# Optimization experiments

Measured on AMD Instinct MI355X. Metric: run time of the kernel, lower is better.

Reference implementation:

```python
import jax, jax.numpy as jnp
import numpy as np

B, DV, DT, H, G, E = 4096, 1024, 1024, 1024, 4096, 8
D = DV + DT  # fused dim = 2048


def setup_inputs() -> dict:
    key = jax.random.key(0)
    ks = jax.random.split(key, 8)
    s = 0.02
    return {
        "vision_cls": jax.random.normal(ks[0], (B, DV), jnp.float32),
        "text_cls": jax.random.normal(ks[1], (B, DT), jnp.float32),
        "W1_imm": jax.random.normal(ks[2], (E, D, H), jnp.float32) * s,
        "b1_imm": jnp.zeros((E, H), jnp.float32),
        "W2_imm": jax.random.normal(ks[3], (E, H, 1), jnp.float32) * s,
        "b2_imm": jnp.zeros((E, 1), jnp.float32),
        "W1_gene": jax.random.normal(ks[4], (E, D, H), jnp.float32) * s,
        "b1_gene": jnp.zeros((E, H), jnp.float32),
        "W2_gene": jax.random.normal(ks[5], (E, H, G), jnp.float32) * s,
        "b2_gene": jnp.zeros((E, G), jnp.float32),
        "organ_idx": jax.random.randint(ks[6], (B,), 0, E, jnp.int32),
    }


def reference(vision_cls, text_cls, W1_imm, b1_imm, W2_imm, b2_imm,
              W1_gene, b1_gene, W2_gene, b2_gene, organ_idx):
    # fused features [B, D]
    fused = jnp.concatenate([vision_cls, text_cls], axis=-1)
    # Dense MoE reference: run every organ head on the full batch, then
    # select each sample's routed output (same math as the per-group
    # gather -> MLP -> scatter in the original; dropout is eval-mode identity).
    h_i = jax.nn.relu(jnp.einsum('bd,edh->ebh', fused, W1_imm) + b1_imm[:, None, :])
    imm_all = jnp.einsum('ebh,eh->eb', h_i, W2_imm[:, :, 0]) + b2_imm[:, :1]  # [E,B]
    h_g = jax.nn.relu(jnp.einsum('bd,edh->ebh', fused, W1_gene) + b1_gene[:, None, :])
    gene_all = jnp.einsum('ebh,ehg->ebg', h_g, W2_gene) + b2_gene[:, None, :]  # [E,B,G]
    bidx = jnp.arange(fused.shape[0])
    immune = imm_all[organ_idx, bidx]      # [B]
    gene = gene_all[organ_idx, bidx]       # [B,G] (uniform gene_dim -> no padding needed)
    return immune, gene, vision_cls, text_cls
```

## Files before the change

kernel.cpp:

```cpp
#include <hip/hip_runtime.h>


#define B_N 4096
#define DV  1024
#define DD  2048
#define HH  1024
#define GG  4096
#define EE  8
#define BM  128
#define MAXRB 40
#define PERM_N (MAXRB * BM)

typedef __bf16 bf16x8 __attribute__((ext_vector_type(8)));
typedef float f32x4 __attribute__((ext_vector_type(4)));
typedef unsigned short u16x4v __attribute__((ext_vector_type(4)));
typedef unsigned short u16x8v __attribute__((ext_vector_type(8)));

#define H_CNT 0
#define H_FIL 8
#define H_OFF 16
#define H_NRB 24
#define H_BLK 32

static __device__ __forceinline__ unsigned short f2bf(float f) {
  return __builtin_bit_cast(unsigned short, (__bf16)f);
}
static __device__ __forceinline__ float bf2f(unsigned short s) {
  return __builtin_bit_cast(float, (unsigned)s << 16);
}
static __device__ __forceinline__ void gload16(const void* g, void* l) {
  __builtin_amdgcn_global_load_lds(
      (const __attribute__((address_space(1))) unsigned int*)g,
      (__attribute__((address_space(3))) unsigned int*)l, 16, 0, 0);
}

__global__ __launch_bounds__(1024) void routing(const int* __restrict__ organ,
                                                int* __restrict__ hdr,
                                                int* __restrict__ perm) {
  __shared__ int cnt[EE], fil[EE], off[EE];
  const int tid = threadIdx.x;
  if (tid < EE) { cnt[tid] = 0; fil[tid] = 0; }
  __syncthreads();
#pragma unroll
  for (int i = 0; i < 4; ++i) atomicAdd(&cnt[organ[tid + (i << 10)]], 1);
#pragma unroll
  for (int i = 0; i < 5; ++i) perm[tid + (i << 10)] = -1;
  __syncthreads();
  if (tid == 0) {
    int acc = 0;
    for (int e = 0; e < EE; ++e) {
      off[e] = acc;
      hdr[H_OFF + e] = acc;
      hdr[H_CNT + e] = cnt[e];
      int nb = (cnt[e] + BM - 1) >> 7;
      int rb0 = acc >> 7;
      for (int i = 0; i < nb; ++i) hdr[H_BLK + rb0 + i] = e;
      acc += nb << 7;
    }
    hdr[H_NRB] = acc >> 7;
  }
  __syncthreads();
#pragma unroll
  for (int i = 0; i < 4; ++i) {
    int b = tid + (i << 10);
    int e = organ[b];
    int slot = off[e] + atomicAdd(&fil[e], 1);
    perm[slot] = b;
  }
}

static __device__ __forceinline__ void abuild_body(
    int bx, const float* __restrict__ vis, const float* __restrict__ txt,
    const int* __restrict__ hdr, const int* __restrict__ perm,
    unsigned short* __restrict__ Abuf) {
  const int nr = hdr[H_NRB] << 7;
  const int tid = threadIdx.x;
  const int c = tid << 3;
  const float* srcbase = (c < DV) ? vis : txt;
  const int cc = (c < DV) ? c : c - DV;
#pragma unroll
  for (int p = 0; p < 4; ++p) {
    int r = (bx << 2) + p;
    if (r >= nr) return;
    int smp = perm[r];
    u16x8v v;
    if (smp >= 0) {
      const float* src = srcbase + (size_t)smp * 1024 + cc;
      float4 a = *(const float4*)src, b = *(const float4*)(src + 4);
      v[0] = f2bf(a.x); v[1] = f2bf(a.y); v[2] = f2bf(a.z); v[3] = f2bf(a.w);
      v[4] = f2bf(b.x); v[5] = f2bf(b.y); v[6] = f2bf(b.z); v[7] = f2bf(b.w);
    } else {
#pragma unroll
      for (int i = 0; i < 8; ++i) v[i] = 0;
    }
    *(u16x8v*)&Abuf[(size_t)r * DD + c] = v;
  }
}

static __device__ __forceinline__ void copy_body(
    int bx, const float4* __restrict__ v, const float4* __restrict__ t,
    float4* __restrict__ ov, float4* __restrict__ ot) {
  const int n4 = B_N * DV / 4;
  for (int i = bx * 256 + (int)threadIdx.x; i < n4; i += 1024 * 256) {
    ov[i] = v[i];
    ot[i] = t[i];
  }
}

__global__ __launch_bounds__(256) void k_A(
    const float* __restrict__ vis, const float* __restrict__ txt,
    const int* __restrict__ hdr, const int* __restrict__ perm,
    unsigned short* __restrict__ Abuf, float4* __restrict__ ov,
    float4* __restrict__ ot) {
  int bx = blockIdx.x;
  if (bx < PERM_N / 4) { abuild_body(bx, vis, txt, hdr, perm, Abuf); return; }
  bx -= PERM_N / 4;
  copy_body(bx, (const float4*)vis, (const float4*)txt, ov, ot);
}

template <int KDIM, int NST>
static __device__ __forceinline__ void gemm_core(
    const unsigned short* __restrict__ Aseg,
    const float* __restrict__ Bglob,
    unsigned short* smem, f32x4 (&acc)[4][4]) {
  const int tid = threadIdx.x;
  const int lane = tid & 63;
  const int wr = ((tid >> 6) >> 1) << 6, wc = ((tid >> 6) & 1) << 6;
  const int lr = lane & 15, lk = (lane >> 4) << 3;
  const int arow = tid >> 2, akq = (tid & 3) << 3;
  const int wbase = (tid & 192) << 3;
  const int bn = tid & 127, bkh = tid >> 7;
  const int bs3 = (bn ^ (bn >> 3)) & 7;
  constexpr int NT = KDIM / 32;

  float bv[16];

  auto issueA = [&](int buf, int k0) {
    gload16(Aseg + (size_t)arow * KDIM + k0 + akq, smem + (buf << 12) + wbase);
    gload16(Aseg + (size_t)(64 + arow) * KDIM + k0 + akq,
            smem + (buf << 12) + 2048 + wbase);
  };
  auto issueB = [&](int k0) {
    const float* p = Bglob + (size_t)(k0 + (bkh << 4)) * NST + bn;
#pragma unroll
    for (int i = 0; i < 16; ++i) bv[i] = p[(size_t)i * NST];
  };
  auto writeB = [&](int buf) {
    unsigned short* row = smem + 8192 + (buf << 12) + (bn << 5);
#pragma unroll
    for (int j = 0; j < 4; ++j) {
      u16x4v w;
      w[0] = f2bf(bv[4 * j + 0]);
      w[1] = f2bf(bv[4 * j + 1]);
      w[2] = f2bf(bv[4 * j + 2]);
      w[3] = f2bf(bv[4 * j + 3]);
      *(u16x4v*)(row + ((((bkh << 2) + j) ^ bs3) << 2)) = w;
    }
  };

  issueA(0, 0);
  issueB(0);
  writeB(0);
  asm volatile("s_waitcnt vmcnt(0)" ::: "memory");
  __syncthreads();

#pragma unroll 2
  for (int kt = 0; kt < NT; ++kt) {
    const int cur = kt & 1;
    if (kt + 1 < NT) {
      issueA(cur ^ 1, (kt + 1) << 5);
      issueB((kt + 1) << 5);
    }
    bf16x8 af[4], bfr[4];
#pragma unroll
    for (int m = 0; m < 4; ++m)
      af[m] = *(const bf16x8*)&smem[(cur << 12) + (wr + m * 16 + lr) * 32 + lk];
#pragma unroll
    for (int n = 0; n < 4; ++n) {
      const int fr = wc + n * 16 + lr;
      const int s3 = (fr ^ (fr >> 3)) & 7;
      const unsigned short* row = smem + 8192 + (cur << 12) + (fr << 5);
      const int g = (lane >> 4) << 1;
      union { unsigned long long q[2]; bf16x8 v; } u;
      u.q[0] = *(const unsigned long long*)(row + ((g ^ s3) << 2));
      u.q[1] = *(const unsigned long long*)(row + (((g + 1) ^ s3) << 2));
      bfr[n] = u.v;
    }
#pragma unroll
    for (int m = 0; m < 4; ++m)
#pragma unroll
      for (int n = 0; n < 4; ++n)
        acc[m][n] = __builtin_amdgcn_mfma_f32_16x16x32_bf16(af[m], bfr[n], acc[m][n], 0, 0, 0);
    if (kt + 1 < NT) writeB(cur ^ 1);
    asm volatile("s_waitcnt vmcnt(0)" ::: "memory");
    __syncthreads();
  }
}

__global__ __launch_bounds__(256) void k_L1(
    const unsigned short* __restrict__ Abuf, const float* __restrict__ W1i,
    const float* __restrict__ W1g, const float* __restrict__ b1i,
    const float* __restrict__ b1g, const int* __restrict__ hdr,
    unsigned short* __restrict__ H1, unsigned short* __restrict__ H2) {
  __shared__ __align__(16) unsigned short smem[16384];
  const int bx = blockIdx.x;
  const int rb = bx >> 4;
  if (rb >= hdr[H_NRB]) return;
  const int sub = bx & 15, head = sub >> 3, cb = (sub & 7) << 7;
  const int e = hdr[H_BLK + rb];
  const float* Bglob = (head ? W1g : W1i) + (size_t)e * DD * HH + cb;
  const float* bias = (head ? b1g : b1i) + e * HH;
  unsigned short* Hout = head ? H2 : H1;
  const int tid = threadIdx.x;
  const int lane = tid & 63, wave = tid >> 6;
  const int wr = (wave >> 1) << 6, wc = (wave & 1) << 6;
  const int lr = lane & 15;

  f32x4 acc[4][4];
#pragma unroll
  for (int m = 0; m < 4; ++m)
#pragma unroll
    for (int n = 0; n < 4; ++n) acc[m][n] = (f32x4){0.f, 0.f, 0.f, 0.f};

  gemm_core<DD, HH>(Abuf + (size_t)rb * BM * DD, Bglob, smem, acc);

  const int r0l = wr + ((lane >> 4) << 2);
#pragma unroll
  for (int n = 0; n < 4; ++n) {
    const int col = wc + n * 16 + lr;
    const float bv = bias[cb + col];
#pragma unroll
    for (int m = 0; m < 4; ++m)
#pragma unroll
      for (int v = 0; v < 4; ++v) {
        int row = r0l + m * 16 + v;
        float x = acc[m][n][v] + bv;
        x = x > 0.f ? x : 0.f;
        smem[((row << 7) + col) ^ ((row & 7) << 3)] = f2bf(x);
      }
  }
  __syncthreads();
#pragma unroll
  for (int c = 0; c < 8; ++c) {
    int q = c * 256 + tid;
    int row = q >> 4, ch = q & 15;
    int off = ((row << 7) + (ch << 3)) ^ ((row & 7) << 3);
    u16x8v val = *(const u16x8v*)&smem[off];
    *(u16x8v*)&Hout[(size_t)(rb * BM + row) * HH + cb + (ch << 3)] = val;
  }
}

static __device__ __forceinline__ void immune_body(
    int bx, const int* __restrict__ hdr, const int* __restrict__ perm,
    const unsigned short* __restrict__ H1, const float* __restrict__ W2,
    const float* __restrict__ b2, float* __restrict__ out) {
  const int nrb = hdr[H_NRB];
  const int r = bx * 4 + (threadIdx.x >> 6);
  if (r >= nrb * BM) return;
  const int b = perm[r];
  if (b < 0) return;
  const int e = hdr[H_BLK + (r >> 7)];
  const int lane = threadIdx.x & 63;
  const unsigned short* h = H1 + (size_t)r * HH + lane * 16;
  const float* w = W2 + (size_t)e * HH + lane * 16;
  float s = 0.f;
#pragma unroll
  for (int i = 0; i < 16; ++i) s += bf2f(h[i]) * w[i];
#pragma unroll
  for (int off = 32; off >= 1; off >>= 1) s += __shfl_xor(s, off, 64);
  if (lane == 0) out[b] = s + b2[e];
}

#define G_L2 (MAXRB * 32)
__global__ __launch_bounds__(256) void k_L2(
    const unsigned short* __restrict__ H2buf, const float* __restrict__ W2g,
    const float* __restrict__ b2g, const int* __restrict__ hdr,
    const int* __restrict__ perm, float* __restrict__ outg,
    const unsigned short* __restrict__ H1, const float* __restrict__ W2i,
    const float* __restrict__ b2i, float* __restrict__ outi) {
  __shared__ __align__(16) unsigned short smem[16384];
  int bx = blockIdx.x;
  if (bx >= G_L2) {
    immune_body(bx - G_L2, hdr, perm, H1, W2i, b2i, outi);
    return;
  }
  const int rb = bx % MAXRB;
  const int cb = (bx / MAXRB) << 7;
  if (rb >= hdr[H_NRB]) return;
  const int e = hdr[H_BLK + rb];
  const float* Bglob = W2g + (size_t)e * HH * GG + cb;
  const int tid = threadIdx.x;
  const int lane = tid & 63, wave = tid >> 6;
  const int wr = (wave >> 1) << 6, wc = (wave & 1) << 6;
  const int lr = lane & 15;

  f32x4 acc[4][4];
#pragma unroll
  for (int m = 0; m < 4; ++m)
#pragma unroll
    for (int n = 0; n < 4; ++n) acc[m][n] = (f32x4){0.f, 0.f, 0.f, 0.f};

  gemm_core<HH, GG>(H2buf + (size_t)rb * BM * HH, Bglob, smem, acc);

  const int r0l = wr + ((lane >> 4) << 2);
#pragma unroll
  for (int n = 0; n < 4; ++n) {
    const int col = wc + n * 16 + lr;
    const float bv = b2g[e * GG + cb + col];
#pragma unroll
    for (int m = 0; m < 4; ++m)
#pragma unroll
      for (int v = 0; v < 4; ++v) {
        int row = r0l + m * 16 + v;
        smem[((row << 7) + col) ^ ((row & 7) << 3)] = f2bf(acc[m][n][v] + bv);
      }
  }
  __syncthreads();
#pragma unroll
  for (int c = 0; c < 8; ++c) {
    int q = c * 256 + tid;
    int row = q >> 4, ch = q & 15;
    int sm = perm[rb * BM + row];
    if (sm < 0) continue;
    int off = ((row << 7) + (ch << 3)) ^ ((row & 7) << 3);
    u16x8v val = *(const u16x8v*)&smem[off];
    float4 f0, f1;
    f0.x = bf2f(val[0]); f0.y = bf2f(val[1]); f0.z = bf2f(val[2]); f0.w = bf2f(val[3]);
    f1.x = bf2f(val[4]); f1.y = bf2f(val[5]); f1.z = bf2f(val[6]); f1.w = bf2f(val[7]);
    float* dst = outg + (size_t)sm * GG + cb + (ch << 3);
    *(float4*)dst = f0;
    *(float4*)(dst + 4) = f1;
  }
}

extern "C" void kernel_launch(void* const* d_in, const int* in_sizes, int n_in,
                              void* d_out, int out_size, void* d_ws, size_t ws_size,
                              hipStream_t stream) {
  (void)in_sizes; (void)n_in; (void)out_size; (void)ws_size;
  const float* vis = (const float*)d_in[0];
  const float* txt = (const float*)d_in[1];
  const float* W1i = (const float*)d_in[2];
  const float* b1i = (const float*)d_in[3];
  const float* W2i = (const float*)d_in[4];
  const float* b2i = (const float*)d_in[5];
  const float* W1g = (const float*)d_in[6];
  const float* b1g = (const float*)d_in[7];
  const float* W2g = (const float*)d_in[8];
  const float* b2g = (const float*)d_in[9];
  const int* organ = (const int*)d_in[10];

  float* out_imm = (float*)d_out;
  float* out_gene = out_imm + B_N;
  float* out_vis = out_gene + (size_t)B_N * GG;
  float* out_txt = out_vis + (size_t)B_N * DV;

  int* hdr = (int*)d_ws;
  int* perm = hdr + 128;

  const size_t OFF_ABUF = 32768;
  const size_t OFF_H1 = OFF_ABUF + (size_t)PERM_N * DD * 2;
  const size_t OFF_H2 = OFF_H1 + (size_t)PERM_N * HH * 2;
  unsigned short* Abuf = (unsigned short*)((char*)d_ws + OFF_ABUF);
  unsigned short* H1 = (unsigned short*)((char*)d_ws + OFF_H1);
  unsigned short* H2 = (unsigned short*)((char*)d_ws + OFF_H2);

  routing<<<1, 1024, 0, stream>>>(organ, hdr, perm);
  k_A<<<PERM_N / 4 + 1024, 256, 0, stream>>>(vis, txt, hdr, perm, Abuf,
                                             (float4*)out_vis, (float4*)out_txt);
  k_L1<<<MAXRB * 16, 256, 0, stream>>>(Abuf, W1i, W1g, b1i, b1g, hdr, H1, H2);
  k_L2<<<G_L2 + PERM_N / 4, 256, 0, stream>>>(H2, W2g, b2g, hdr, perm, out_gene,
                                              H1, W2i, b2i, out_imm);
}
```

Before: 283.0 us.

## Deepen GEMM prefetch with register double-buffered B, swizzled A, block remap

Restructures the GEMM main loop so B tiles are fetched two K-steps ahead into alternating register buffers using float4 loads, and relaxes waits to vmcnt(4) so global loads stay in flight across barriers. It also XOR-swizzles A's LDS layout to reduce bank conflicts, and remaps block indices so consecutive blocks share the same expert weight column tile for better L2 reuse. The vis/txt output copy moves from the A-build kernel into the L1 kernel so it overlaps with GEMM work. The cost is more registers, hand-tuned waitcnt counts that must match the load count exactly, and an extra barrier before the epilogue.

```diff
diff --git a/kernel.cpp b/kernel.cpp
--- a/kernel.cpp
+++ b/kernel.cpp
@@ -69,10 +69,11 @@
   }
 }
 
-static __device__ __forceinline__ void abuild_body(
-    int bx, const float* __restrict__ vis, const float* __restrict__ txt,
+__global__ __launch_bounds__(256) void k_A(
+    const float* __restrict__ vis, const float* __restrict__ txt,
     const int* __restrict__ hdr, const int* __restrict__ perm,
     unsigned short* __restrict__ Abuf) {
+  const int bx = blockIdx.x;
   const int nr = hdr[H_NRB] << 7;
   const int tid = threadIdx.x;
   const int c = tid << 3;
@@ -107,17 +108,6 @@
   }
 }
 
-__global__ __launch_bounds__(256) void k_A(
-    const float* __restrict__ vis, const float* __restrict__ txt,
-    const int* __restrict__ hdr, const int* __restrict__ perm,
-    unsigned short* __restrict__ Abuf, float4* __restrict__ ov,
-    float4* __restrict__ ot) {
-  int bx = blockIdx.x;
-  if (bx < PERM_N / 4) { abuild_body(bx, vis, txt, hdr, perm, Abuf); return; }
-  bx -= PERM_N / 4;
-  copy_body(bx, (const float4*)vis, (const float4*)txt, ov, ot);
-}
-
 template <int KDIM, int NST>
 static __device__ __forceinline__ void gemm_core(
     const unsigned short* __restrict__ Aseg,
@@ -126,60 +116,54 @@
   const int tid = threadIdx.x;
   const int lane = tid & 63;
   const int wr = ((tid >> 6) >> 1) << 6, wc = ((tid >> 6) & 1) << 6;
-  const int lr = lane & 15, lk = (lane >> 4) << 3;
-  const int arow = tid >> 2, akq = (tid & 3) << 3;
+  const int lr = lane & 15;
+  const int arow = tid >> 2;
+  const int kq_src = (((tid & 3) ^ ((arow >> 1) & 3)) << 3);
   const int wbase = (tid & 192) << 3;
-  const int bn = tid & 127, bkh = tid >> 7;
-  const int bs3 = (bn ^ (bn >> 3)) & 7;
+  const int bn4 = (tid & 31) << 2;
+  const int bk4 = (tid >> 5) << 2;
   constexpr int NT = KDIM / 32;
 
-  float bv[16];
+  float4 bvA[4], bvB[4];
 
   auto issueA = [&](int buf, int k0) {
-    gload16(Aseg + (size_t)arow * KDIM + k0 + akq, smem + (buf << 12) + wbase);
-    gload16(Aseg + (size_t)(64 + arow) * KDIM + k0 + akq,
+    gload16(Aseg + (size_t)arow * KDIM + k0 + kq_src, smem + (buf << 12) + wbase);
+    gload16(Aseg + (size_t)(64 + arow) * KDIM + k0 + kq_src,
             smem + (buf << 12) + 2048 + wbase);
   };
-  auto issueB = [&](int k0) {
-    const float* p = Bglob + (size_t)(k0 + (bkh << 4)) * NST + bn;
-#pragma unroll
-    for (int i = 0; i < 16; ++i) bv[i] = p[(size_t)i * NST];
+  auto issueB = [&](float4 (&bv)[4], int k0) {
+    const float* p = Bglob + (size_t)(k0 + bk4) * NST + bn4;
+#pragma unroll
+    for (int i = 0; i < 4; ++i) bv[i] = *(const float4*)(p + (size_t)i * NST);
   };
-  auto writeB = [&](int buf) {
-    unsigned short* row = smem + 8192 + (buf << 12) + (bn << 5);
+  auto writeB = [&](int buf, float4 (&bv)[4]) {
+    const float* f0 = (const float*)&bv[0];
+    const float* f1 = (const float*)&bv[1];
+    const float* f2 = (const float*)&bv[2];
+    const float* f3 = (const float*)&bv[3];
 #pragma unroll
     for (int j = 0; j < 4; ++j) {
+      const int n = bn4 + j;
+      const int s3 = (n ^ (n >> 3)) & 7;
       u16x4v w;
-      w[0] = f2bf(bv[4 * j + 0]);
-      w[1] = f2bf(bv[4 * j + 1]);
-      w[2] = f2bf(bv[4 * j + 2]);
-      w[3] = f2bf(bv[4 * j + 3]);
-      *(u16x4v*)(row + ((((bkh << 2) + j) ^ bs3) << 2)) = w;
+      w[0] = f2bf(f0[j]); w[1] = f2bf(f1[j]);
+      w[2] = f2bf(f2[j]); w[3] = f2bf(f3[j]);
+      *(u16x4v*)(smem + 8192 + (buf << 12) + (n << 5) + ((((bk4 >> 2)) ^ s3) << 2)) = w;
     }
   };
-
-  issueA(0, 0);
-  issueB(0);
-  writeB(0);
-  asm volatile("s_waitcnt vmcnt(0)" ::: "memory");
-  __syncthreads();
-
-#pragma unroll 2
-  for (int kt = 0; kt < NT; ++kt) {
-    const int cur = kt & 1;
-    if (kt + 1 < NT) {
-      issueA(cur ^ 1, (kt + 1) << 5);
-      issueB((kt + 1) << 5);
-    }
+  auto compute = [&](int buf) {
     bf16x8 af[4], bfr[4];
 #pragma unroll
-    for (int m = 0; m < 4; ++m)
-      af[m] = *(const bf16x8*)&smem[(cur << 12) + (wr + m * 16 + lr) * 32 + lk];
+    for (int m = 0; m < 4; ++m) {
+      const int r = wr + m * 16 + lr;
+      const int cs = ((lane >> 4) ^ ((r >> 1) & 3)) << 3;
+      af[m] = *(const bf16x8*)&smem[(buf << 12) + r * 32 + cs];
+    }
 #pragma unroll
     for (int n = 0; n < 4; ++n) {
       const int fr = wc + n * 16 + lr;
       const int s3 = (fr ^ (fr >> 3)) & 7;
-      const unsigned short* row = smem + 8192 + (cur << 12) + (fr << 5);
+      const unsigned short* row = smem + 8192 + (buf << 12) + (fr << 5);
       const int g = (lane >> 4) << 1;
       union { unsigned long long q[2]; bf16x8 v; } u;
       u.q[0] = *(const unsigned long long*)(row + ((g ^ s3) << 2));
@@ -191,22 +175,56 @@
 #pragma unroll
       for (int n = 0; n < 4; ++n)
         acc[m][n] = __builtin_amdgcn_mfma_f32_16x16x32_bf16(af[m], bfr[n], acc[m][n], 0, 0, 0);
-    if (kt + 1 < NT) writeB(cur ^ 1);
-    asm volatile("s_waitcnt vmcnt(0)" ::: "memory");
-    __syncthreads();
-  }
-}
-
+  };
+
+  issueB(bvA, 0);
+  writeB(0, bvA);
+  issueA(0, 0);
+  __builtin_amdgcn_sched_barrier(0);
+  issueB(bvB, 1 << 5);
+  asm volatile("s_waitcnt vmcnt(4) lgkmcnt(0)" ::: "memory");
+  __builtin_amdgcn_s_barrier();
+
+  int t = 0;
+  for (; t + 2 < NT; t += 2) {
+    issueA(1, (t + 1) << 5);
+    __builtin_amdgcn_sched_barrier(0);
+    issueB(bvA, (t + 2) << 5);
+    compute(0);
+    writeB(1, bvB);
+    asm volatile("s_waitcnt vmcnt(4) lgkmcnt(0)" ::: "memory");
+    __builtin_amdgcn_s_barrier();
+    issueA(0, (t + 2) << 5);
+    __builtin_amdgcn_sched_barrier(0);
+    issueB(bvB, (t + 3) << 5);
+    compute(1);
+    writeB(0, bvA);
+    asm volatile("s_waitcnt vmcnt(4) lgkmcnt(0)" ::: "memory");
+    __builtin_amdgcn_s_barrier();
+  }
+  issueA(1, (NT - 1) << 5);
+  compute(0);
+  writeB(1, bvB);
+  asm volatile("s_waitcnt vmcnt(0) lgkmcnt(0)" ::: "memory");
+  __builtin_amdgcn_s_barrier();
+  compute(1);
+}
+
+#define G_L1 (MAXRB * 16)
 __global__ __launch_bounds__(256) void k_L1(
     const unsigned short* __restrict__ Abuf, const float* __restrict__ W1i,
     const float* __restrict__ W1g, const float* __restrict__ b1i,
     const float* __restrict__ b1g, const int* __restrict__ hdr,
-    unsigned short* __restrict__ H1, unsigned short* __restrict__ H2) {
+    unsigned short* __restrict__ H1, unsigned short* __restrict__ H2,
+    const float4* __restrict__ vis4, const float4* __restrict__ txt4,
+    float4* __restrict__ ov, float4* __restrict__ ot) {
   __shared__ __align__(16) unsigned short smem[16384];
-  const int bx = blockIdx.x;
-  const int rb = bx >> 4;
+  int bx = blockIdx.x;
+  if (bx >= G_L1) { copy_body(bx - G_L1, vis4, txt4, ov, ot); return; }
+  const int id = (bx & 7) * (G_L1 >> 3) + (bx >> 3);
+  const int rb = id % MAXRB;
   if (rb >= hdr[H_NRB]) return;
-  const int sub = bx & 15, head = sub >> 3, cb = (sub & 7) << 7;
+  const int sub = id / MAXRB, head = sub >> 3, cb = (sub & 7) << 7;
   const int e = hdr[H_BLK + rb];
   const float* Bglob = (head ? W1g : W1i) + (size_t)e * DD * HH + cb;
   const float* bias = (head ? b1g : b1i) + e * HH;
@@ -223,6 +241,7 @@
     for (int n = 0; n < 4; ++n) acc[m][n] = (f32x4){0.f, 0.f, 0.f, 0.f};
 
   gemm_core<DD, HH>(Abuf + (size_t)rb * BM * DD, Bglob, smem, acc);
+  __syncthreads();
 
   const int r0l = wr + ((lane >> 4) << 2);
 #pragma unroll
@@ -284,9 +303,10 @@
     immune_body(bx - G_L2, hdr, perm, H1, W2i, b2i, outi);
     return;
   }
-  const int rb = bx % MAXRB;
-  const int cb = (bx / MAXRB) << 7;
+  const int id = (bx & 7) * (G_L2 >> 3) + (bx >> 3);
+  const int rb = id % MAXRB;
   if (rb >= hdr[H_NRB]) return;
+  const int cb = (id / MAXRB) << 7;
   const int e = hdr[H_BLK + rb];
   const float* Bglob = W2g + (size_t)e * HH * GG + cb;
   const int tid = threadIdx.x;
@@ -301,6 +321,7 @@
     for (int n = 0; n < 4; ++n) acc[m][n] = (f32x4){0.f, 0.f, 0.f, 0.f};
 
   gemm_core<HH, GG>(H2buf + (size_t)rb * BM * HH, Bglob, smem, acc);
+  __syncthreads();
 
   const int r0l = wr + ((lane >> 4) << 2);
 #pragma unroll
@@ -365,9 +386,10 @@
   unsigned short* H2 = (unsigned short*)((char*)d_ws + OFF_H2);
 
   routing<<<1, 1024, 0, stream>>>(organ, hdr, perm);
-  k_A<<<PERM_N / 4 + 1024, 256, 0, stream>>>(vis, txt, hdr, perm, Abuf,
-                                             (float4*)out_vis, (float4*)out_txt);
-  k_L1<<<MAXRB * 16, 256, 0, stream>>>(Abuf, W1i, W1g, b1i, b1g, hdr, H1, H2);
+  k_A<<<PERM_N / 4, 256, 0, stream>>>(vis, txt, hdr, perm, Abuf);
+  k_L1<<<G_L1 + 1024, 256, 0, stream>>>(Abuf, W1i, W1g, b1i, b1g, hdr, H1, H2,
+                                        (const float4*)vis, (const float4*)txt,
+                                        (float4*)out_vis, (float4*)out_txt);
   k_L2<<<G_L2 + PERM_N / 4, 256, 0, stream>>>(H2, W2g, b2g, hdr, perm, out_gene,
                                               H1, W2i, b2i, out_imm);
 }
```

After: 259.0 us. -8.5%, faster.
